# Kernel tuning notes

Measured on AMD Instinct MI355X. Metric: run time of the kernel, lower is better.

The kernel has to match this reference:

```python
import jax, jax.numpy as jnp
import numpy as np

N = 50000      # nodes
E = 800000     # edges (avg degree 16)
F_IN = 256     # input features
H = 128        # hidden
C = 40         # classes


def setup_inputs() -> dict:
    key = jax.random.key(0)
    ks = jax.random.split(key, 10)
    features = jax.random.normal(ks[0], (N, F_IN), dtype=jnp.float32)
    src = jax.random.randint(ks[1], (E,), 0, N, dtype=jnp.int32)
    dst = jax.random.randint(ks[2], (E,), 0, N, dtype=jnp.int32)
    edge_weights = jax.random.uniform(ks[3], (E,), dtype=jnp.float32)
    def glorot(k, i, o):
        return jax.random.normal(k, (i, o), dtype=jnp.float32) * np.float32(1.0 / np.sqrt(i))
    W1 = glorot(ks[4], F_IN, H); b1 = jnp.zeros((H,), jnp.float32)
    W2 = glorot(ks[5], H, H);    b2 = jnp.zeros((H,), jnp.float32)
    W3 = glorot(ks[6], H, C);    b3 = jnp.zeros((C,), jnp.float32)
    return dict(features=features, src=src, dst=dst, edge_weights=edge_weights,
                W1=W1, b1=b1, W2=W2, b2=b2, W3=W3, b3=b3)


def _gcn_layer(h, src, dst, ew, out_norm, in_norm, W, b, act):
    # norm='both': pre-scale by out_degree^-0.5, post-scale by in_degree^-0.5
    h = h * out_norm[:, None]
    in_gt_out = W.shape[0] > W.shape[1]
    if in_gt_out:
        h = h @ W                      # matmul first (in_feats > out_feats)
    # message = u_mul_e, reduce = sum  (SpMM-style gather-scale-scatter)
    agg = jax.ops.segment_sum(h[src] * ew[:, None], dst, num_segments=N)
    if not in_gt_out:
        agg = agg @ W                  # aggregate first (in_feats <= out_feats)
    agg = agg * in_norm[:, None] + b
    return act(agg) if act is not None else agg


def reference(features, src, dst, edge_weights, W1, b1, W2, b2, W3, b3):
    ones = jnp.ones((E,), jnp.float32)
    out_deg = jnp.clip(jax.ops.segment_sum(ones, src, num_segments=N), 1.0)
    in_deg = jnp.clip(jax.ops.segment_sum(ones, dst, num_segments=N), 1.0)
    out_norm = out_deg ** -0.5
    in_norm = in_deg ** -0.5
    relu = jax.nn.relu
    # dropout is identity in eval mode
    h = _gcn_layer(features, src, dst, edge_weights, out_norm, in_norm, W1, b1, relu)
    h = _gcn_layer(h, src, dst, edge_weights, out_norm, in_norm, W2, b2, relu)
    h = _gcn_layer(h, src, dst, edge_weights, out_norm, in_norm, W3, b3, None)
    return h
```

## Files before the change

### kernel.cpp

```cpp
#include <hip/hip_runtime.h>
#include <hip/hip_bf16.h>
#include <cstdint>


#define F_IN 256
#define HDIM 128
#define CDIM 40
#define RBITS 13
#define RSIZE 8192
#define NSUB 64

__global__ __launch_bounds__(256)
void histo_range(const int* __restrict__ src, const int* __restrict__ dst,
                 int* __restrict__ pc, int E) {
    __shared__ int h[RSIZE];
    const int s = blockIdx.x;
    const int r = blockIdx.y;
    const int base = r << RBITS;
    const int t = threadIdx.x;
    int4* h4 = reinterpret_cast<int4*>(h);
    for (int j = t; j < RSIZE / 4; j += 256) h4[j] = make_int4(0, 0, 0, 0);
    __syncthreads();

    const int ech = (E + NSUB - 1) / NSUB;
    const int e0 = s * ech;
    const int e1 = min(E, e0 + ech);
    const int n4 = (e1 - e0) >> 2;
    for (int g = t; g < n4; g += 256) {
        int4 d4 = *reinterpret_cast<const int4*>(dst + e0 + g * 4);
        int4 s4 = *reinterpret_cast<const int4*>(src + e0 + g * 4);
        #pragma unroll
        for (int j = 0; j < 4; ++j) {
            int d = (&d4.x)[j] - base;
            int v = (&s4.x)[j] - base;
            if ((unsigned)d < RSIZE) atomicAdd(&h[d], 1);
            if ((unsigned)v < RSIZE) atomicAdd(&h[v], 0x10000);
        }
    }
    for (int e = e0 + n4 * 4 + t; e < e1; e += 256) {
        int d = dst[e] - base, v = src[e] - base;
        if ((unsigned)d < RSIZE) atomicAdd(&h[d], 1);
        if ((unsigned)v < RSIZE) atomicAdd(&h[v], 0x10000);
    }
    __syncthreads();
    int* p = pc + ((size_t)r * NSUB + s) * RSIZE;
    for (int j = t; j < RSIZE; j += 256) p[j] = h[j];
}

__global__ __launch_bounds__(256)
void scan_blocks(const int* __restrict__ pc, int* __restrict__ out,
                 int* __restrict__ bsums, int n) {
    const int t = threadIdx.x;
    const int idx = blockIdx.x * 1024 + t * 4;
    int4 v = make_int4(0, 0, 0, 0);
    if (idx + 3 < n) {
        const int r = idx >> RBITS, off = idx & (RSIZE - 1);
        const int* p = pc + (size_t)r * NSUB * RSIZE + off;
        #pragma unroll 8
        for (int c = 0; c < NSUB; ++c) {
            int4 u = *reinterpret_cast<const int4*>(p + (size_t)c * RSIZE);
            v.x += u.x & 0xffff; v.y += u.y & 0xffff;
            v.z += u.z & 0xffff; v.w += u.w & 0xffff;
        }
    } else {
        for (int j = 0; j < 4; ++j) {
            if (idx + j < n) {
                const int r = (idx + j) >> RBITS, off = (idx + j) & (RSIZE - 1);
                int s = 0;
                for (int c = 0; c < NSUB; ++c)
                    s += pc[(size_t)r * NSUB * RSIZE + (size_t)c * RSIZE + off] & 0xffff;
                (&v.x)[j] = s;
            }
        }
    }
    const int s = v.x + v.y + v.z + v.w;
    const int lane = t & 63;
    int incl = s;
    #pragma unroll
    for (int off = 1; off < 64; off <<= 1) {
        int u = __shfl_up(incl, off);
        if (lane >= off) incl += u;
    }
    __shared__ int wsum[4];
    if (lane == 63) wsum[t >> 6] = incl;
    __syncthreads();
    const int w = t >> 6;
    int woff = 0;
    if (w > 0) woff += wsum[0];
    if (w > 1) woff += wsum[1];
    if (w > 2) woff += wsum[2];
    const int excl = woff + incl - s;
    if (idx + 3 < n) {
        *reinterpret_cast<int4*>(out + idx) =
            make_int4(excl, excl + v.x, excl + v.x + v.y, excl + v.x + v.y + v.z);
    } else {
        if (idx     < n) out[idx]     = excl;
        if (idx + 1 < n) out[idx + 1] = excl + v.x;
        if (idx + 2 < n) out[idx + 2] = excl + v.x + v.y;
        if (idx + 3 < n) out[idx + 3] = excl + v.x + v.y + v.z;
    }
    if (t == 255) bsums[blockIdx.x] = woff + incl;
}

__global__ __launch_bounds__(64)
void scan_sums(int* __restrict__ bsums, int nb) {
    const int lane = threadIdx.x & 63;
    int carry = 0;
    for (int base = 0; base < nb; base += 64) {
        int v = (base + lane < nb) ? bsums[base + lane] : 0;
        int incl = v;
        #pragma unroll
        for (int off = 1; off < 64; off <<= 1) {
            int u = __shfl_up(incl, off);
            if (lane >= off) incl += u;
        }
        if (base + lane < nb) bsums[base + lane] = carry + incl - v;
        carry += __shfl(incl, 63);
    }
}

__global__ __launch_bounds__(256)
void node_prep_kernel(const int* __restrict__ pc,
                      int* __restrict__ row_ptr, const int* __restrict__ bsums,
                      float* __restrict__ out_norm, float* __restrict__ in_norm,
                      int* __restrict__ cb, int n, int E) {
    int i = blockIdx.x * 256 + threadIdx.x;
    if (i < n) {
        const int r = i >> RBITS, off = i & (RSIZE - 1);
        const int* p = pc + (size_t)r * NSUB * RSIZE + off;
        int rp = row_ptr[i] + bsums[i >> 10];
        row_ptr[i] = rp;
        int cur = rp;
        int od = 0;
        #pragma unroll 8
        for (int c = 0; c < NSUB; ++c) {
            unsigned pv = (unsigned)p[(size_t)c * RSIZE];
            cb[(size_t)c * n + i] = cur;
            cur += (int)(pv & 0xffffu);
            od  += (int)(pv >> 16);
        }
        int id = cur - rp;
        out_norm[i] = rsqrtf((float)max(od, 1));
        in_norm[i]  = rsqrtf((float)max(id, 1));
    }
    if (i == 0) row_ptr[n] = E;
}

__global__ __launch_bounds__(256)
void scatter_range(const int* __restrict__ src, const int* __restrict__ dst,
                   const float* __restrict__ ew, const float* __restrict__ out_norm,
                   const int* __restrict__ cb, int2* __restrict__ edges,
                   int E, int N) {
    __shared__ int cur[RSIZE];
    const int s = blockIdx.x;
    const int r = blockIdx.y;
    const int base = r << RBITS;
    const int t = threadIdx.x;
    for (int j = t; j < RSIZE; j += 256)
        if (base + j < N) cur[j] = cb[(size_t)s * N + base + j];
    __syncthreads();

    const int ech = (E + NSUB - 1) / NSUB;
    const int e0 = s * ech;
    const int e1 = min(E, e0 + ech);
    const int n4 = (e1 - e0) >> 2;
    for (int g = t; g < n4; g += 256) {
        int4 d4 = *reinterpret_cast<const int4*>(dst + e0 + g * 4);
        int4 s4 = *reinterpret_cast<const int4*>(src + e0 + g * 4);
        float4 w4 = *reinterpret_cast<const float4*>(ew + e0 + g * 4);
        #pragma unroll
        for (int j = 0; j < 4; ++j) {
            int d = (&d4.x)[j] - base;
            if ((unsigned)d < RSIZE) {
                int sv = (&s4.x)[j];
                int pos = atomicAdd(&cur[d], 1);
                float w = (&w4.x)[j] * out_norm[sv];
                edges[pos] = make_int2(sv, __float_as_int(w));
            }
        }
    }
    for (int e = e0 + n4 * 4 + t; e < e1; e += 256) {
        int d = dst[e] - base;
        if ((unsigned)d < RSIZE) {
            int sv = src[e];
            int pos = atomicAdd(&cur[d], 1);
            float w = ew[e] * out_norm[sv];
            edges[pos] = make_int2(sv, __float_as_int(w));
        }
    }
}

template <int MODE>
__global__ __launch_bounds__(256)
void gemm128_f32(const float* __restrict__ A, const float* __restrict__ B,
                 float* __restrict__ C, int M, int K,
                 const float* __restrict__ rownorm, const float* __restrict__ bias) {
    constexpr int BM = 64, BK = 16;
    __shared__ float As[BK][BM + 4];
    __shared__ float Bs[BK][128];

    const int t = threadIdx.x;
    const int row0 = blockIdx.x * BM;
    const int rowbase = (t >> 4) * 4;
    const int colbase = (t & 15) * 4;
    const int ar  = t >> 2;
    const int akq = (t & 3) * 4;
    const int bk  = t >> 4;
    const int bc4 = (t & 15) * 4;

    float acc0[4][4], acc1[4][4];
    #pragma unroll
    for (int i = 0; i < 4; ++i)
        #pragma unroll
        for (int j = 0; j < 4; ++j) { acc0[i][j] = 0.f; acc1[i][j] = 0.f; }

    const bool arow_ok = (row0 + ar < M);
    const float* ap = A + (size_t)(row0 + ar) * K + akq;

    float4 a0 = make_float4(0.f, 0.f, 0.f, 0.f);
    if (arow_ok) a0 = *reinterpret_cast<const float4*>(ap);
    const float* bp = B + (size_t)bk * 128;
    float4 b0 = *reinterpret_cast<const float4*>(bp + bc4);
    float4 b1 = *reinterpret_cast<const float4*>(bp + 64 + bc4);

    for (int k0 = 0; k0 < K; k0 += BK) {
        __syncthreads();
        As[akq + 0][ar] = a0.x;
        As[akq + 1][ar] = a0.y;
        As[akq + 2][ar] = a0.z;
        As[akq + 3][ar] = a0.w;
        *reinterpret_cast<float4*>(&Bs[bk][bc4])      = b0;
        *reinterpret_cast<float4*>(&Bs[bk][64 + bc4]) = b1;
        __syncthreads();

        if (k0 + BK < K) {
            if (arow_ok) a0 = *reinterpret_cast<const float4*>(ap + k0 + BK);
            const float* bp2 = B + (size_t)(k0 + BK + bk) * 128;
            b0 = *reinterpret_cast<const float4*>(bp2 + bc4);
            b1 = *reinterpret_cast<const float4*>(bp2 + 64 + bc4);
        }

        #pragma unroll
        for (int kk = 0; kk < BK; ++kk) {
            float4 av  = *reinterpret_cast<const float4*>(&As[kk][rowbase]);
            float4 bv0 = *reinterpret_cast<const float4*>(&Bs[kk][colbase]);
            float4 bv1 = *reinterpret_cast<const float4*>(&Bs[kk][64 + colbase]);
            float a[4]   = {av.x, av.y, av.z, av.w};
            float b0a[4] = {bv0.x, bv0.y, bv0.z, bv0.w};
            float b1a[4] = {bv1.x, bv1.y, bv1.z, bv1.w};
            #pragma unroll
            for (int i = 0; i < 4; ++i) {
                #pragma unroll
                for (int j = 0; j < 4; ++j) {
                    acc0[i][j] = fmaf(a[i], b0a[j], acc0[i][j]);
                    acc1[i][j] = fmaf(a[i], b1a[j], acc1[i][j]);
                }
            }
        }
    }

    float4 bb0 = make_float4(0.f, 0.f, 0.f, 0.f), bb1 = bb0;
    if (MODE == 1) {
        bb0 = *reinterpret_cast<const float4*>(bias + colbase);
        bb1 = *reinterpret_cast<const float4*>(bias + 64 + colbase);
    }
    #pragma unroll
    for (int i = 0; i < 4; ++i) {
        int row = row0 + rowbase + i;
        if (row >= M) break;
        float4 v0 = make_float4(acc0[i][0], acc0[i][1], acc0[i][2], acc0[i][3]);
        float4 v1 = make_float4(acc1[i][0], acc1[i][1], acc1[i][2], acc1[i][3]);
        if (MODE == 1) {
            float rn = rownorm[row];
            v0.x = fmaxf(fmaf(v0.x, rn, bb0.x), 0.f);
            v0.y = fmaxf(fmaf(v0.y, rn, bb0.y), 0.f);
            v0.z = fmaxf(fmaf(v0.z, rn, bb0.z), 0.f);
            v0.w = fmaxf(fmaf(v0.w, rn, bb0.w), 0.f);
            v1.x = fmaxf(fmaf(v1.x, rn, bb1.x), 0.f);
            v1.y = fmaxf(fmaf(v1.y, rn, bb1.y), 0.f);
            v1.z = fmaxf(fmaf(v1.z, rn, bb1.z), 0.f);
            v1.w = fmaxf(fmaf(v1.w, rn, bb1.w), 0.f);
        }
        float* cp = C + (size_t)row * 128 + colbase;
        *reinterpret_cast<float4*>(cp)      = v0;
        *reinterpret_cast<float4*>(cp + 64) = v1;
    }
}

template <int MODE>
__global__ __launch_bounds__(256)
void gemm_f32(const float* __restrict__ A, const float* __restrict__ B,
              float* __restrict__ C, int M, int Nn, int K,
              int lda, int ldb, int ldc,
              const float* __restrict__ rownorm, const float* __restrict__ bias) {
    constexpr int BM = 64, BN = 64, BK = 16;
    __shared__ float As[BK][BM + 4];
    __shared__ float Bs[BK][BN];

    const int t = threadIdx.x;
    const int row0 = blockIdx.x * BM;
    const int col0 = blockIdx.y * BN;
    const int rowbase = (t >> 4) * 4;
    const int colbase = (t & 15) * 4;
    const int ar  = t >> 2;
    const int akq = (t & 3) * 4;
    const int bk  = t >> 4;
    const int bc4 = (t & 15) * 4;

    float acc[4][4];
    #pragma unroll
    for (int i = 0; i < 4; ++i)
        #pragma unroll
        for (int j = 0; j < 4; ++j) acc[i][j] = 0.f;

    const bool arow_ok = (row0 + ar < M);
    const bool bcol_ok = (col0 + bc4 < Nn);
    const float* ap = A + (size_t)(row0 + ar) * lda + akq;

    float4 a0 = make_float4(0.f, 0.f, 0.f, 0.f), bv = a0;
    if (arow_ok) a0 = *reinterpret_cast<const float4*>(ap);
    if (bcol_ok)
        bv = *reinterpret_cast<const float4*>(B + (size_t)bk * ldb + col0 + bc4);

    for (int k0 = 0; k0 < K; k0 += BK) {
        __syncthreads();
        As[akq + 0][ar] = a0.x;
        As[akq + 1][ar] = a0.y;
        As[akq + 2][ar] = a0.z;
        As[akq + 3][ar] = a0.w;
        *reinterpret_cast<float4*>(&Bs[bk][bc4]) = bv;
        __syncthreads();

        if (k0 + BK < K) {
            if (arow_ok) a0 = *reinterpret_cast<const float4*>(ap + k0 + BK);
            if (bcol_ok)
                bv = *reinterpret_cast<const float4*>(B + (size_t)(k0 + BK + bk) * ldb + col0 + bc4);
        }

        #pragma unroll
        for (int kk = 0; kk < BK; ++kk) {
            float4 av  = *reinterpret_cast<const float4*>(&As[kk][rowbase]);
            float4 bv2 = *reinterpret_cast<const float4*>(&Bs[kk][colbase]);
            float a[4] = {av.x, av.y, av.z, av.w};
            float b[4] = {bv2.x, bv2.y, bv2.z, bv2.w};
            #pragma unroll
            for (int i = 0; i < 4; ++i)
                #pragma unroll
                for (int j = 0; j < 4; ++j)
                    acc[i][j] = fmaf(a[i], b[j], acc[i][j]);
        }
    }

    if (col0 + colbase >= Nn) return;
    float4 bb = make_float4(0.f, 0.f, 0.f, 0.f);
    if (MODE == 1) bb = *reinterpret_cast<const float4*>(bias + col0 + colbase);
    #pragma unroll
    for (int i = 0; i < 4; ++i) {
        int row = row0 + rowbase + i;
        if (row >= M) break;
        float4 v = make_float4(acc[i][0], acc[i][1], acc[i][2], acc[i][3]);
        if (MODE == 1) {
            float rn = rownorm[row];
            v.x = fmaxf(fmaf(v.x, rn, bb.x), 0.f);
            v.y = fmaxf(fmaf(v.y, rn, bb.y), 0.f);
            v.z = fmaxf(fmaf(v.z, rn, bb.z), 0.f);
            v.w = fmaxf(fmaf(v.w, rn, bb.w), 0.f);
        }
        *reinterpret_cast<float4*>(C + (size_t)row * ldc + col0 + colbase) = v;
    }
}

template <int EPI>
__global__ __launch_bounds__(256)
void spmm128(const float* __restrict__ H, const int* __restrict__ row_ptr,
             const int2* __restrict__ edges,
             float* __restrict__ out, const float* __restrict__ in_norm,
             const float* __restrict__ bias, int n) {
    int wid  = (blockIdx.x * 256 + threadIdx.x) >> 6;
    int lane = threadIdx.x & 63;
    if (wid >= n) return;
    const int quarter = lane >> 4;
    const int q       = lane & 15;
    int e0 = row_ptr[wid], e1 = row_ptr[wid + 1];
    float4 acc0 = make_float4(0.f, 0.f, 0.f, 0.f);
    float4 acc1 = make_float4(0.f, 0.f, 0.f, 0.f);
    #pragma unroll 2
    for (int e = e0 + quarter; e < e1; e += 4) {
        int2 er = edges[e];
        int   s = er.x;
        float w = __int_as_float(er.y);
        const float* hp = H + (size_t)s * 128 + q * 4;
        float4 v0 = *reinterpret_cast<const float4*>(hp);
        float4 v1 = *reinterpret_cast<const float4*>(hp + 64);
        acc0.x = fmaf(w, v0.x, acc0.x); acc0.y = fmaf(w, v0.y, acc0.y);
        acc0.z = fmaf(w, v0.z, acc0.z); acc0.w = fmaf(w, v0.w, acc0.w);
        acc1.x = fmaf(w, v1.x, acc1.x); acc1.y = fmaf(w, v1.y, acc1.y);
        acc1.z = fmaf(w, v1.z, acc1.z); acc1.w = fmaf(w, v1.w, acc1.w);
    }
    #pragma unroll
    for (int d = 16; d <= 32; d <<= 1) {
        acc0.x += __shfl_xor(acc0.x, d); acc0.y += __shfl_xor(acc0.y, d);
        acc0.z += __shfl_xor(acc0.z, d); acc0.w += __shfl_xor(acc0.w, d);
        acc1.x += __shfl_xor(acc1.x, d); acc1.y += __shfl_xor(acc1.y, d);
        acc1.z += __shfl_xor(acc1.z, d); acc1.w += __shfl_xor(acc1.w, d);
    }
    if (quarter == 0) {
        if (EPI == 1) {
            float nn = in_norm[wid];
            float4 bb0 = *reinterpret_cast<const float4*>(bias + q * 4);
            float4 bb1 = *reinterpret_cast<const float4*>(bias + 64 + q * 4);
            acc0.x = fmaxf(fmaf(acc0.x, nn, bb0.x), 0.f);
            acc0.y = fmaxf(fmaf(acc0.y, nn, bb0.y), 0.f);
            acc0.z = fmaxf(fmaf(acc0.z, nn, bb0.z), 0.f);
            acc0.w = fmaxf(fmaf(acc0.w, nn, bb0.w), 0.f);
            acc1.x = fmaxf(fmaf(acc1.x, nn, bb1.x), 0.f);
            acc1.y = fmaxf(fmaf(acc1.y, nn, bb1.y), 0.f);
            acc1.z = fmaxf(fmaf(acc1.z, nn, bb1.z), 0.f);
            acc1.w = fmaxf(fmaf(acc1.w, nn, bb1.w), 0.f);
        }
        float* op = out + (size_t)wid * 128 + q * 4;
        *reinterpret_cast<float4*>(op)      = acc0;
        *reinterpret_cast<float4*>(op + 64) = acc1;
    }
}

__global__ __launch_bounds__(256)
void spmm40(const float* __restrict__ H, const int* __restrict__ row_ptr,
            const int2* __restrict__ edges,
            float* __restrict__ out, const float* __restrict__ in_norm,
            const float* __restrict__ bias, int n) {
    int wid  = (blockIdx.x * 256 + threadIdx.x) >> 6;
    int lane = threadIdx.x & 63;
    if (wid >= n) return;
    const int quarter = lane >> 4;
    const int q       = lane & 15;
    int e0 = row_ptr[wid], e1 = row_ptr[wid + 1];
    float4 acc = make_float4(0.f, 0.f, 0.f, 0.f);
    #pragma unroll 2
    for (int e = e0 + quarter; e < e1; e += 4) {
        int2 er = edges[e];
        int   s = er.x;
        float w = __int_as_float(er.y);
        float4 v = *reinterpret_cast<const float4*>(H + (size_t)s * 64 + q * 4);
        acc.x = fmaf(w, v.x, acc.x);
        acc.y = fmaf(w, v.y, acc.y);
        acc.z = fmaf(w, v.z, acc.z);
        acc.w = fmaf(w, v.w, acc.w);
    }
    #pragma unroll
    for (int d = 16; d <= 32; d <<= 1) {
        acc.x += __shfl_xor(acc.x, d);
        acc.y += __shfl_xor(acc.y, d);
        acc.z += __shfl_xor(acc.z, d);
        acc.w += __shfl_xor(acc.w, d);
    }
    if (quarter == 0 && q * 4 < CDIM) {
        float nn = in_norm[wid];
        float4 bb = *reinterpret_cast<const float4*>(bias + q * 4);
        acc.x = fmaf(acc.x, nn, bb.x);
        acc.y = fmaf(acc.y, nn, bb.y);
        acc.z = fmaf(acc.z, nn, bb.z);
        acc.w = fmaf(acc.w, nn, bb.w);
        *reinterpret_cast<float4*>(out + (size_t)wid * CDIM + q * 4) = acc;
    }
}


extern "C" void kernel_launch(void* const* d_in, const int* in_sizes, int n_in,
                              void* d_out, int out_size, void* d_ws, size_t ws_size,
                              hipStream_t stream) {
    const float* features = (const float*)d_in[0];
    const int*   src      = (const int*)d_in[1];
    const int*   dst      = (const int*)d_in[2];
    const float* ew       = (const float*)d_in[3];
    const float* W1       = (const float*)d_in[4];
    const float* b1       = (const float*)d_in[5];
    const float* W2       = (const float*)d_in[6];
    const float* b2       = (const float*)d_in[7];
    const float* W3       = (const float*)d_in[8];
    const float* b3       = (const float*)d_in[9];
    float* out = (float*)d_out;

    const int N = in_sizes[0] / F_IN;
    const int E = in_sizes[1];
    const int NR = (N + RSIZE - 1) >> RBITS;

    char* ws = (char*)d_ws;
    size_t off = 0;
    auto alloc = [&](size_t bytes) -> void* {
        void* p = ws + off;
        off += (bytes + 255) & ~(size_t)255;
        return p;
    };
    int*   row_ptr  = (int*)alloc((size_t)(N + 1) * 4);
    float* out_norm = (float*)alloc((size_t)N * 4);
    float* in_norm  = (float*)alloc((size_t)N * 4);
    int2*  edges    = (int2*)alloc((size_t)E * 8);
    float* B0       = (float*)alloc((size_t)N * HDIM * 4);
    float* B1       = (float*)alloc((size_t)N * HDIM * 4);
    float* B2       = (float*)alloc((size_t)N * HDIM * 4);
    const int nb    = (N + 1023) / 1024;
    int*   bsums    = (int*)alloc((size_t)nb * 4);
    int*   pc       = (int*)B0;
    int*   cb       = (int*)B1;
    (void)ws_size;

    {
        dim3 grid(NSUB, NR);
        histo_range<<<grid, 256, 0, stream>>>(src, dst, pc, E);
    }
    scan_blocks<<<nb, 256, 0, stream>>>(pc, row_ptr, bsums, N);
    scan_sums<<<1, 64, 0, stream>>>(bsums, nb);
    int ngrid = (N + 255) / 256;
    node_prep_kernel<<<ngrid, 256, 0, stream>>>(pc, row_ptr, bsums,
                                                out_norm, in_norm, cb, N, E);
    {
        dim3 grid(NSUB, NR);
        scatter_range<<<grid, 256, 0, stream>>>(src, dst, ew, out_norm, cb,
                                                edges, E, N);
    }

    const int spmm_grid = (N + 3) / 4;
    const int ggrid = (N + 63) / 64;

    gemm128_f32<0><<<ggrid, 256, 0, stream>>>(features, W1, B0, N, F_IN,
                                              nullptr, nullptr);
    spmm128<1><<<spmm_grid, 256, 0, stream>>>(B0, row_ptr, edges, B1, in_norm, b1, N);

    spmm128<0><<<spmm_grid, 256, 0, stream>>>(B1, row_ptr, edges, B2, nullptr, nullptr, N);
    gemm128_f32<1><<<ggrid, 256, 0, stream>>>(B2, W2, B0, N, HDIM, in_norm, b2);

    {
        dim3 grid(ggrid, 1);
        gemm_f32<0><<<grid, 256, 0, stream>>>(B0, W3, B1, N, CDIM, HDIM,
                                              HDIM, CDIM, 64, nullptr, nullptr);
    }
    spmm40<<<spmm_grid, 256, 0, stream>>>(B1, row_ptr, edges, out, in_norm, b3, N);
}
```

Measured before the change: 289.4 us.

## Replace FP32 SIMT GEMMs with split-bf16 MFMA GEMMs for layers one and two

Measured after the change: 250.1 us. 13.6% less time.

```diff
diff --git a/kernel.cpp b/kernel.cpp
--- a/kernel.cpp
+++ b/kernel.cpp
@@ -9,6 +9,17 @@
 #define RBITS 13
 #define RSIZE 8192
 #define NSUB 64
+
+typedef short bf16x8 __attribute__((ext_vector_type(8)));
+typedef float f32x4  __attribute__((ext_vector_type(4)));
+
+__device__ __forceinline__ ushort f2bf(float x) {
+    uint b = __float_as_uint(x);
+    return (ushort)((b + 0x7fffu + ((b >> 16) & 1u)) >> 16);
+}
+__device__ __forceinline__ float bf2f(ushort h) {
+    return __uint_as_float(((uint)h) << 16);
+}
 
 __global__ __launch_bounds__(256)
 void histo_range(const int* __restrict__ src, const int* __restrict__ dst,
@@ -190,100 +201,116 @@
     }
 }
 
+__global__ __launch_bounds__(256)
+void conv_w(const float* __restrict__ W, ushort* __restrict__ Wt_hi,
+            ushort* __restrict__ Wt_lo, int K) {
+    int i = blockIdx.x * 256 + threadIdx.x;
+    if (i < K * 128) {
+        int k = i >> 7, n = i & 127;
+        float x = W[i];
+        ushort hi = f2bf(x);
+        ushort lo = f2bf(x - bf2f(hi));
+        Wt_hi[(size_t)n * K + k] = hi;
+        Wt_lo[(size_t)n * K + k] = lo;
+    }
+}
+
 template <int MODE>
 __global__ __launch_bounds__(256)
-void gemm128_f32(const float* __restrict__ A, const float* __restrict__ B,
-                 float* __restrict__ C, int M, int K,
-                 const float* __restrict__ rownorm, const float* __restrict__ bias) {
-    constexpr int BM = 64, BK = 16;
-    __shared__ float As[BK][BM + 4];
-    __shared__ float Bs[BK][128];
+void gemm128_mfma(const float* __restrict__ A, const ushort* __restrict__ Wt_hi,
+                  const ushort* __restrict__ Wt_lo, float* __restrict__ C,
+                  int M, int K,
+                  const float* __restrict__ rownorm, const float* __restrict__ bias) {
+    constexpr int BK = 32;
+    constexpr int AP = 40;
+    __shared__ __align__(16) ushort As_hi[64 * AP];
+    __shared__ __align__(16) ushort As_lo[64 * AP];
+    __shared__ __align__(16) ushort Bs_hi[128 * AP];
+    __shared__ __align__(16) ushort Bs_lo[128 * AP];
 
     const int t = threadIdx.x;
-    const int row0 = blockIdx.x * BM;
-    const int rowbase = (t >> 4) * 4;
-    const int colbase = (t & 15) * 4;
-    const int ar  = t >> 2;
-    const int akq = (t & 3) * 4;
-    const int bk  = t >> 4;
-    const int bc4 = (t & 15) * 4;
-
-    float acc0[4][4], acc1[4][4];
-    #pragma unroll
-    for (int i = 0; i < 4; ++i)
-        #pragma unroll
-        for (int j = 0; j < 4; ++j) { acc0[i][j] = 0.f; acc1[i][j] = 0.f; }
+    const int w = t >> 6;
+    const int l = t & 63;
+    const int row0 = blockIdx.x * 64;
+
+    const int ar = t >> 2;
+    const int ak = (t & 3) * 8;
+    const int bn = t >> 1;
+    const int bko = (t & 1) * 16;
+
+    const int fr = l & 15;
+    const int fk = (l >> 4) * 8;
+
+    f32x4 acc[8];
+    #pragma unroll
+    for (int i = 0; i < 8; ++i) acc[i] = (f32x4){0.f, 0.f, 0.f, 0.f};
 
     const bool arow_ok = (row0 + ar < M);
-    const float* ap = A + (size_t)(row0 + ar) * K + akq;
-
-    float4 a0 = make_float4(0.f, 0.f, 0.f, 0.f);
-    if (arow_ok) a0 = *reinterpret_cast<const float4*>(ap);
-    const float* bp = B + (size_t)bk * 128;
-    float4 b0 = *reinterpret_cast<const float4*>(bp + bc4);
-    float4 b1 = *reinterpret_cast<const float4*>(bp + 64 + bc4);
+    const float* ap = A + (size_t)(row0 + ar) * K;
 
     for (int k0 = 0; k0 < K; k0 += BK) {
+        float av[8];
+        if (arow_ok) {
+            float4 f0 = *reinterpret_cast<const float4*>(ap + k0 + ak);
+            float4 f1 = *reinterpret_cast<const float4*>(ap + k0 + ak + 4);
+            av[0] = f0.x; av[1] = f0.y; av[2] = f0.z; av[3] = f0.w;
+            av[4] = f1.x; av[5] = f1.y; av[6] = f1.z; av[7] = f1.w;
+        } else {
+            #pragma unroll
+            for (int j = 0; j < 8; ++j) av[j] = 0.f;
+        }
+        bf16x8 ah, al;
+        #pragma unroll
+        for (int j = 0; j < 8; ++j) {
+            ushort hi = f2bf(av[j]);
+            ah[j] = (short)hi;
+            al[j] = (short)f2bf(av[j] - bf2f(hi));
+        }
+        const ushort* wh = Wt_hi + (size_t)bn * K + k0 + bko;
+        const ushort* wl = Wt_lo + (size_t)bn * K + k0 + bko;
+        bf16x8 bh0 = *reinterpret_cast<const bf16x8*>(wh);
+        bf16x8 bh1 = *reinterpret_cast<const bf16x8*>(wh + 8);
+        bf16x8 bl0 = *reinterpret_cast<const bf16x8*>(wl);
+        bf16x8 bl1 = *reinterpret_cast<const bf16x8*>(wl + 8);
+
         __syncthreads();
-        As[akq + 0][ar] = a0.x;
-        As[akq + 1][ar] = a0.y;
-        As[akq + 2][ar] = a0.z;
-        As[akq + 3][ar] = a0.w;
-        *reinterpret_cast<float4*>(&Bs[bk][bc4])      = b0;
-        *reinterpret_cast<float4*>(&Bs[bk][64 + bc4]) = b1;
+        *reinterpret_cast<bf16x8*>(As_hi + ar * AP + ak) = ah;
+        *reinterpret_cast<bf16x8*>(As_lo + ar * AP + ak) = al;
+        *reinterpret_cast<bf16x8*>(Bs_hi + bn * AP + bko)     = bh0;
+        *reinterpret_cast<bf16x8*>(Bs_hi + bn * AP + bko + 8) = bh1;
+        *reinterpret_cast<bf16x8*>(Bs_lo + bn * AP + bko)     = bl0;
+        *reinterpret_cast<bf16x8*>(Bs_lo + bn * AP + bko + 8) = bl1;
         __syncthreads();
 
-        if (k0 + BK < K) {
-            if (arow_ok) a0 = *reinterpret_cast<const float4*>(ap + k0 + BK);
-            const float* bp2 = B + (size_t)(k0 + BK + bk) * 128;
-            b0 = *reinterpret_cast<const float4*>(bp2 + bc4);
-            b1 = *reinterpret_cast<const float4*>(bp2 + 64 + bc4);
-        }
-
-        #pragma unroll
-        for (int kk = 0; kk < BK; ++kk) {
-            float4 av  = *reinterpret_cast<const float4*>(&As[kk][rowbase]);
-            float4 bv0 = *reinterpret_cast<const float4*>(&Bs[kk][colbase]);
-            float4 bv1 = *reinterpret_cast<const float4*>(&Bs[kk][64 + colbase]);
-            float a[4]   = {av.x, av.y, av.z, av.w};
-            float b0a[4] = {bv0.x, bv0.y, bv0.z, bv0.w};
-            float b1a[4] = {bv1.x, bv1.y, bv1.z, bv1.w};
-            #pragma unroll
-            for (int i = 0; i < 4; ++i) {
-                #pragma unroll
-                for (int j = 0; j < 4; ++j) {
-                    acc0[i][j] = fmaf(a[i], b0a[j], acc0[i][j]);
-                    acc1[i][j] = fmaf(a[i], b1a[j], acc1[i][j]);
-                }
-            }
-        }
-    }
-
-    float4 bb0 = make_float4(0.f, 0.f, 0.f, 0.f), bb1 = bb0;
+        bf16x8 a_hi = *reinterpret_cast<const bf16x8*>(As_hi + (w * 16 + fr) * AP + fk);
+        bf16x8 a_lo = *reinterpret_cast<const bf16x8*>(As_lo + (w * 16 + fr) * AP + fk);
+        #pragma unroll
+        for (int nt = 0; nt < 8; ++nt) {
+            bf16x8 b_hi = *reinterpret_cast<const bf16x8*>(Bs_hi + (nt * 16 + fr) * AP + fk);
+            bf16x8 b_lo = *reinterpret_cast<const bf16x8*>(Bs_lo + (nt * 16 + fr) * AP + fk);
+            acc[nt] = __builtin_amdgcn_mfma_f32_16x16x32_bf16(a_hi, b_hi, acc[nt], 0, 0, 0);
+            acc[nt] = __builtin_amdgcn_mfma_f32_16x16x32_bf16(a_hi, b_lo, acc[nt], 0, 0, 0);
+            acc[nt] = __builtin_amdgcn_mfma_f32_16x16x32_bf16(a_lo, b_hi, acc[nt], 0, 0, 0);
+        }
+    }
+
+    float bb[8];
     if (MODE == 1) {
-        bb0 = *reinterpret_cast<const float4*>(bias + colbase);
-        bb1 = *reinterpret_cast<const float4*>(bias + 64 + colbase);
-    }
-    #pragma unroll
-    for (int i = 0; i < 4; ++i) {
-        int row = row0 + rowbase + i;
-        if (row >= M) break;
-        float4 v0 = make_float4(acc0[i][0], acc0[i][1], acc0[i][2], acc0[i][3]);
-        float4 v1 = make_float4(acc1[i][0], acc1[i][1], acc1[i][2], acc1[i][3]);
-        if (MODE == 1) {
-            float rn = rownorm[row];
-            v0.x = fmaxf(fmaf(v0.x, rn, bb0.x), 0.f);
-            v0.y = fmaxf(fmaf(v0.y, rn, bb0.y), 0.f);
-            v0.z = fmaxf(fmaf(v0.z, rn, bb0.z), 0.f);
-            v0.w = fmaxf(fmaf(v0.w, rn, bb0.w), 0.f);
-            v1.x = fmaxf(fmaf(v1.x, rn, bb1.x), 0.f);
-            v1.y = fmaxf(fmaf(v1.y, rn, bb1.y), 0.f);
-            v1.z = fmaxf(fmaf(v1.z, rn, bb1.z), 0.f);
-            v1.w = fmaxf(fmaf(v1.w, rn, bb1.w), 0.f);
-        }
-        float* cp = C + (size_t)row * 128 + colbase;
-        *reinterpret_cast<float4*>(cp)      = v0;
-        *reinterpret_cast<float4*>(cp + 64) = v1;
+        #pragma unroll
+        for (int nt = 0; nt < 8; ++nt) bb[nt] = bias[nt * 16 + fr];
+    }
+    #pragma unroll
+    for (int r = 0; r < 4; ++r) {
+        int row = row0 + w * 16 + (l >> 4) * 4 + r;
+        if (row >= M) continue;
+        float rn = (MODE == 1) ? rownorm[row] : 0.f;
+        float* cp = C + (size_t)row * 128;
+        #pragma unroll
+        for (int nt = 0; nt < 8; ++nt) {
+            float v = acc[nt][r];
+            if (MODE == 1) v = fmaxf(fmaf(v, rn, bb[nt]), 0.f);
+            cp[nt * 16 + fr] = v;
+        }
     }
 }
 
@@ -492,23 +519,29 @@
         off += (bytes + 255) & ~(size_t)255;
         return p;
     };
-    int*   row_ptr  = (int*)alloc((size_t)(N + 1) * 4);
-    float* out_norm = (float*)alloc((size_t)N * 4);
-    float* in_norm  = (float*)alloc((size_t)N * 4);
-    int2*  edges    = (int2*)alloc((size_t)E * 8);
-    float* B0       = (float*)alloc((size_t)N * HDIM * 4);
-    float* B1       = (float*)alloc((size_t)N * HDIM * 4);
-    float* B2       = (float*)alloc((size_t)N * HDIM * 4);
-    const int nb    = (N + 1023) / 1024;
-    int*   bsums    = (int*)alloc((size_t)nb * 4);
-    int*   pc       = (int*)B0;
-    int*   cb       = (int*)B1;
+    int*    row_ptr  = (int*)alloc((size_t)(N + 1) * 4);
+    float*  out_norm = (float*)alloc((size_t)N * 4);
+    float*  in_norm  = (float*)alloc((size_t)N * 4);
+    int2*   edges    = (int2*)alloc((size_t)E * 8);
+    float*  B0       = (float*)alloc((size_t)N * HDIM * 4);
+    float*  B1       = (float*)alloc((size_t)N * HDIM * 4);
+    float*  B2       = (float*)alloc((size_t)N * HDIM * 4);
+    const int nb     = (N + 1023) / 1024;
+    int*    bsums    = (int*)alloc((size_t)nb * 4);
+    ushort* Wt1_hi   = (ushort*)alloc((size_t)F_IN * 128 * 2);
+    ushort* Wt1_lo   = (ushort*)alloc((size_t)F_IN * 128 * 2);
+    ushort* Wt2_hi   = (ushort*)alloc((size_t)HDIM * 128 * 2);
+    ushort* Wt2_lo   = (ushort*)alloc((size_t)HDIM * 128 * 2);
+    int*    pc       = (int*)B0;
+    int*    cb       = (int*)B1;
     (void)ws_size;
 
     {
         dim3 grid(NSUB, NR);
         histo_range<<<grid, 256, 0, stream>>>(src, dst, pc, E);
     }
+    conv_w<<<(F_IN * 128 + 255) / 256, 256, 0, stream>>>(W1, Wt1_hi, Wt1_lo, F_IN);
+    conv_w<<<(HDIM * 128 + 255) / 256, 256, 0, stream>>>(W2, Wt2_hi, Wt2_lo, HDIM);
     scan_blocks<<<nb, 256, 0, stream>>>(pc, row_ptr, bsums, N);
     scan_sums<<<1, 64, 0, stream>>>(bsums, nb);
     int ngrid = (N + 255) / 256;
@@ -523,12 +556,13 @@
     const int spmm_grid = (N + 3) / 4;
     const int ggrid = (N + 63) / 64;
 
-    gemm128_f32<0><<<ggrid, 256, 0, stream>>>(features, W1, B0, N, F_IN,
-                                              nullptr, nullptr);
+    gemm128_mfma<0><<<ggrid, 256, 0, stream>>>(features, Wt1_hi, Wt1_lo, B0,
+                                               N, F_IN, nullptr, nullptr);
     spmm128<1><<<spmm_grid, 256, 0, stream>>>(B0, row_ptr, edges, B1, in_norm, b1, N);
 
     spmm128<0><<<spmm_grid, 256, 0, stream>>>(B1, row_ptr, edges, B2, nullptr, nullptr, N);
-    gemm128_f32<1><<<ggrid, 256, 0, stream>>>(B2, W2, B0, N, HDIM, in_norm, b2);
+    gemm128_mfma<1><<<ggrid, 256, 0, stream>>>(B2, Wt2_hi, Wt2_lo, B0,
+                                               N, HDIM, in_norm, b2);
 
     {
         dim3 grid(ggrid, 1);
```
